# Optimization experiments

Hardware: AMD Instinct MI355X
Metric: run time of the kernel (lower is better)

## Reference

```python
import jax, jax.numpy as jnp
import numpy as np

N = 4194304  # batch of 2-D points
N_NODE = 16
N_INT = 5


def setup_inputs() -> dict:
    key = jax.random.key(0)
    k1, k2, k3, k4 = jax.random.split(key, 4)
    # Kaiming-ish small init so ReLU chain doesn't blow up
    x = jax.random.normal(k1, (N, 2), dtype=jnp.float32)
    w_in = jax.random.normal(k2, (N_NODE, 2), dtype=jnp.float32) * (1.0 / np.sqrt(2.0))
    w_mid = jax.random.normal(k3, (N_INT, N_NODE, N_NODE), dtype=jnp.float32) * (1.0 / np.sqrt(N_NODE))
    w_out = jax.random.normal(k4, (2, N_NODE), dtype=jnp.float32) * (1.0 / np.sqrt(N_NODE))
    return {"x": x, "w_in": w_in, "w_mid": w_mid, "w_out": w_out}


def reference(x, w_in, w_mid, w_out):
    # Linear(2,16,bias=False) + ReLU
    h = jax.nn.relu(x @ w_in.T)  # [N, 16]
    def step(h, w):
        return jax.nn.relu(h @ w.T), None
    h, _ = jax.lax.scan(step, h, w_mid)
    # final Linear(16,2,bias=False), no activation
    return h @ w_out.T  # [N, 2]
```

## Files before the change

kernel.cpp:

```cpp
#include <hip/hip_runtime.h>


typedef _Float16 h8 __attribute__((ext_vector_type(8)));
typedef float f16v __attribute__((ext_vector_type(16)));
typedef float f4 __attribute__((ext_vector_type(4)));
typedef float f2 __attribute__((ext_vector_type(2)));
typedef unsigned int u32;
typedef u32 u4v __attribute__((ext_vector_type(4)));

static __device__ __forceinline__ f16v mfma32(h8 a, h8 b, f16v c) {
    return __builtin_amdgcn_mfma_f32_32x32x16_f16(a, b, c, 0, 0, 0);
}

static __device__ __forceinline__ u32 cvtpk(float a, float b) {
    return __builtin_bit_cast(u32, __builtin_amdgcn_cvt_pkrtz(a, b));
}

static __device__ __forceinline__ h8 pack4(u32 a, u32 b, u32 c, u32 d) {
    u4v p = {a, b, c, d};
    return __builtin_bit_cast(h8, p);
}

static __device__ __forceinline__ h8 wfrag(const float* row, int hi) {
    const f4* r4 = (const f4*)row;
    f4 q0 = r4[hi], q1 = r4[hi + 2];
    return pack4(cvtpk(q0.x, q0.y), cvtpk(q0.z, q0.w),
                 cvtpk(q1.x, q1.y), cvtpk(q1.z, q1.w));
}

static __device__ __forceinline__ h8 cvt_relu8(f16v a) {
    h8 hb = pack4(cvtpk(a[0], a[1]), cvtpk(a[2], a[3]),
                  cvtpk(a[4], a[5]), cvtpk(a[6], a[7]));
    const h8 z = {};
    return __builtin_elementwise_max(hb, z);
}

__global__ __launch_bounds__(256, 4) void denoiser_mfma32(
    const f2* __restrict__ x,
    const float* __restrict__ w_in,
    const float* __restrict__ w_mid,
    const float* __restrict__ w_out,
    f2* __restrict__ out,
    int n)
{
    const int lane = threadIdx.x & 63;
    const int m    = lane & 15;
    const int hi   = lane >> 5;
    const int wave = threadIdx.x >> 6;

    const h8 hz = {};

    u32 wxy = cvtpk(w_in[2 * m], w_in[2 * m + 1]);
    h8 wi0 = hi == 0 ? pack4(wxy, 0u, 0u, 0u) : hz;
    h8 wi1 = hi == 1 ? pack4(wxy, 0u, 0u, 0u) : hz;

    h8 wm0 = wfrag(w_mid + 0 * 256 + m * 16, hi);
    h8 wm1 = wfrag(w_mid + 1 * 256 + m * 16, hi);
    h8 wm2 = wfrag(w_mid + 2 * 256 + m * 16, hi);
    h8 wm3 = wfrag(w_mid + 3 * 256 + m * 16, hi);
    h8 wm4 = wfrag(w_mid + 4 * 256 + m * 16, hi);

    h8 wo = m < 2 ? wfrag(w_out + m * 16, hi) : hz;

    f16v z16 = {};
    asm("" : "+v"(z16));

    const int nchunks = (n + 255) >> 8;
    const int stride  = gridDim.x;
    const int nm1     = n - 1;

    auto loadx = [&](int c) -> f2 {
        int pi = c * 256 + wave * 64 + lane;
        return x[pi < n ? pi : nm1];
    };

    auto stream = [&](h8 wi, h8 bin, int sbase) {
        f16v a = mfma32(wi, bin, z16);
        h8 b = cvt_relu8(a);
        a = mfma32(wm0, b, z16);  b = cvt_relu8(a);
        a = mfma32(wm1, b, z16);  b = cvt_relu8(a);
        a = mfma32(wm2, b, z16);  b = cvt_relu8(a);
        a = mfma32(wm3, b, z16);  b = cvt_relu8(a);
        a = mfma32(wm4, b, z16);  b = cvt_relu8(a);
        a = mfma32(wo, b, z16);

        if (lane < 32) {
            int p0 = sbase + lane;
            if (p0 < n) out[p0] = (f2){a[0], a[1]};
        }
    };

    auto body = [&](int c, f2 xy) {
        const int base = c * 256 + wave * 64;
        h8 bin = pack4(cvtpk(xy.x, xy.y), 0u, 0u, 0u);
        stream(wi0, bin, base);
        stream(wi1, bin, base + 32);
    };

    int c = blockIdx.x;
    f2 xyA = loadx(c);
    f2 xyB = loadx(c + stride < nchunks ? c + stride : c);

    for (; c < nchunks; c += 2 * stride) {
        const int cB  = c + stride;
        const int cA2 = c + 2 * stride;
        const int cB2 = c + 3 * stride;

        f2 xyA2 = loadx(cA2 < nchunks ? cA2 : c);
        f2 xyB2 = loadx(cB2 < nchunks ? cB2 : c);

        body(c, xyA);
        if (cB < nchunks) body(cB, xyB);

        xyA = xyA2;
        xyB = xyB2;
    }
}

extern "C" void kernel_launch(void* const* d_in, const int* in_sizes, int n_in,
                              void* d_out, int out_size, void* d_ws, size_t ws_size,
                              hipStream_t stream) {
    const float* x     = (const float*)d_in[0];
    const float* w_in  = (const float*)d_in[1];
    const float* w_mid = (const float*)d_in[2];
    const float* w_out = (const float*)d_in[3];

    int n = in_sizes[0] / 2;
    int nchunks = (n + 255) / 256;
    int blocks = nchunks < 2048 ? nchunks : 2048;

    denoiser_mfma32<<<blocks, 256, 0, stream>>>(
        (const f2*)x, w_in, w_mid, w_out, (f2*)d_out, n);
}
```

Before: 33.98 us.

## Replace grid-stride prefetch loop with one chunk per block launch

```diff
diff --git a/kernel.cpp b/kernel.cpp
--- a/kernel.cpp
+++ b/kernel.cpp
@@ -65,16 +65,16 @@
     f16v z16 = {};
     asm("" : "+v"(z16));
 
-    const int nchunks = (n + 255) >> 8;
-    const int stride  = gridDim.x;
-    const int nm1     = n - 1;
+    const int base = blockIdx.x * 256 + wave * 64;
 
-    auto loadx = [&](int c) -> f2 {
-        int pi = c * 256 + wave * 64 + lane;
-        return x[pi < n ? pi : nm1];
-    };
+    f2 xy;
+    {
+        int pi = base + lane;
+        xy = x[pi < n ? pi : n - 1];
+    }
+    h8 bin = pack4(cvtpk(xy.x, xy.y), 0u, 0u, 0u);
 
-    auto stream = [&](h8 wi, h8 bin, int sbase) {
+    auto stream = [&](h8 wi, int sbase) {
         f16v a = mfma32(wi, bin, z16);
         h8 b = cvt_relu8(a);
         a = mfma32(wm0, b, z16);  b = cvt_relu8(a);
@@ -90,31 +90,8 @@
         }
     };
 
-    auto body = [&](int c, f2 xy) {
-        const int base = c * 256 + wave * 64;
-        h8 bin = pack4(cvtpk(xy.x, xy.y), 0u, 0u, 0u);
-        stream(wi0, bin, base);
-        stream(wi1, bin, base + 32);
-    };
-
-    int c = blockIdx.x;
-    f2 xyA = loadx(c);
-    f2 xyB = loadx(c + stride < nchunks ? c + stride : c);
-
-    for (; c < nchunks; c += 2 * stride) {
-        const int cB  = c + stride;
-        const int cA2 = c + 2 * stride;
-        const int cB2 = c + 3 * stride;
-
-        f2 xyA2 = loadx(cA2 < nchunks ? cA2 : c);
-        f2 xyB2 = loadx(cB2 < nchunks ? cB2 : c);
-
-        body(c, xyA);
-        if (cB < nchunks) body(cB, xyB);
-
-        xyA = xyA2;
-        xyB = xyB2;
-    }
+    stream(wi0, base);
+    stream(wi1, base + 32);
 }
 
 extern "C" void kernel_launch(void* const* d_in, const int* in_sizes, int n_in,
@@ -126,8 +103,7 @@
     const float* w_out = (const float*)d_in[3];
 
     int n = in_sizes[0] / 2;
-    int nchunks = (n + 255) / 256;
-    int blocks = nchunks < 2048 ? nchunks : 2048;
+    int blocks = (n + 255) / 256;
 
     denoiser_mfma32<<<blocks, 256, 0, stream>>>(
         (const f2*)x, w_in, w_mid, w_out, (f2*)d_out, n);
```

New measurement: 51.87 us. 52.6% more time.

## Switch to 16x16x32 MFMA with four independent point streams per wave

Applied to the files above, without the earlier changes.

```diff
diff --git a/kernel.cpp b/kernel.cpp
--- a/kernel.cpp
+++ b/kernel.cpp
@@ -2,14 +2,15 @@
 
 
 typedef _Float16 h8 __attribute__((ext_vector_type(8)));
-typedef float f16v __attribute__((ext_vector_type(16)));
+typedef _Float16 h4v __attribute__((ext_vector_type(4)));
 typedef float f4 __attribute__((ext_vector_type(4)));
 typedef float f2 __attribute__((ext_vector_type(2)));
 typedef unsigned int u32;
+typedef u32 u2v __attribute__((ext_vector_type(2)));
 typedef u32 u4v __attribute__((ext_vector_type(4)));
 
-static __device__ __forceinline__ f16v mfma32(h8 a, h8 b, f16v c) {
-    return __builtin_amdgcn_mfma_f32_32x32x16_f16(a, b, c, 0, 0, 0);
+static __device__ __forceinline__ f4 mfma32k(h8 a, h8 b, f4 c) {
+    return __builtin_amdgcn_mfma_f32_16x16x32_f16(a, b, c, 0, 0, 0);
 }
 
 static __device__ __forceinline__ u32 cvtpk(float a, float b) {
@@ -21,21 +22,22 @@
     return __builtin_bit_cast(h8, p);
 }
 
-static __device__ __forceinline__ h8 wfrag(const float* row, int hi) {
+static __device__ __forceinline__ h8 wfrag(const float* row, int g) {
     const f4* r4 = (const f4*)row;
-    f4 q0 = r4[hi], q1 = r4[hi + 2];
-    return pack4(cvtpk(q0.x, q0.y), cvtpk(q0.z, q0.w),
-                 cvtpk(q1.x, q1.y), cvtpk(q1.z, q1.w));
+    f4 q = r4[g];
+    return pack4(cvtpk(q.x, q.y), cvtpk(q.z, q.w), 0u, 0u);
 }
 
-static __device__ __forceinline__ h8 cvt_relu8(f16v a) {
-    h8 hb = pack4(cvtpk(a[0], a[1]), cvtpk(a[2], a[3]),
-                  cvtpk(a[4], a[5]), cvtpk(a[6], a[7]));
-    const h8 z = {};
-    return __builtin_elementwise_max(hb, z);
+static __device__ __forceinline__ h8 cvt_relu4(f4 a) {
+    u2v c = { cvtpk(a[0], a[1]), cvtpk(a[2], a[3]) };
+    h4v hb = __builtin_bit_cast(h4v, c);
+    const h4v z = {};
+    hb = __builtin_elementwise_max(hb, z);
+    u2v r = __builtin_bit_cast(u2v, hb);
+    return pack4(r.x, r.y, 0u, 0u);
 }
 
-__global__ __launch_bounds__(256, 4) void denoiser_mfma32(
+__global__ __launch_bounds__(256, 4) void denoiser_mfma16k32(
     const f2* __restrict__ x,
     const float* __restrict__ w_in,
     const float* __restrict__ w_mid,
@@ -44,26 +46,34 @@
     int n)
 {
     const int lane = threadIdx.x & 63;
-    const int m    = lane & 15;
-    const int hi   = lane >> 5;
+    const int nn   = lane & 15;
+    const int g    = lane >> 4;
     const int wave = threadIdx.x >> 6;
 
     const h8 hz = {};
 
-    u32 wxy = cvtpk(w_in[2 * m], w_in[2 * m + 1]);
-    h8 wi0 = hi == 0 ? pack4(wxy, 0u, 0u, 0u) : hz;
-    h8 wi1 = hi == 1 ? pack4(wxy, 0u, 0u, 0u) : hz;
+    u32 wxy = cvtpk(w_in[2 * nn], w_in[2 * nn + 1]);
+    h8 wiv = pack4(wxy, 0u, 0u, 0u);
+    h8 wi0 = g == 0 ? wiv : hz;
+    h8 wi1 = g == 1 ? wiv : hz;
+    h8 wi2 = g == 2 ? wiv : hz;
+    h8 wi3 = g == 3 ? wiv : hz;
 
-    h8 wm0 = wfrag(w_mid + 0 * 256 + m * 16, hi);
-    h8 wm1 = wfrag(w_mid + 1 * 256 + m * 16, hi);
-    h8 wm2 = wfrag(w_mid + 2 * 256 + m * 16, hi);
-    h8 wm3 = wfrag(w_mid + 3 * 256 + m * 16, hi);
-    h8 wm4 = wfrag(w_mid + 4 * 256 + m * 16, hi);
+    h8 wm0 = wfrag(w_mid + 0 * 256 + nn * 16, g);
+    h8 wm1 = wfrag(w_mid + 1 * 256 + nn * 16, g);
+    h8 wm2 = wfrag(w_mid + 2 * 256 + nn * 16, g);
+    h8 wm3 = wfrag(w_mid + 3 * 256 + nn * 16, g);
+    h8 wm4 = wfrag(w_mid + 4 * 256 + nn * 16, g);
 
-    h8 wo = m < 2 ? wfrag(w_out + m * 16, hi) : hz;
+    h8 wofull = (nn & 3) < 2 ? wfrag(w_out + (nn & 3) * 16, g) : hz;
+    int tsel = nn >> 2;
+    h8 wo0 = tsel == 0 ? wofull : hz;
+    h8 wo1 = tsel == 1 ? wofull : hz;
+    h8 wo2 = tsel == 2 ? wofull : hz;
+    h8 wo3 = tsel == 3 ? wofull : hz;
 
-    f16v z16 = {};
-    asm("" : "+v"(z16));
+    f4 z4 = {};
+    asm("" : "+v"(z4));
 
     const int nchunks = (n + 255) >> 8;
     const int stride  = gridDim.x;
@@ -74,46 +84,57 @@
         return x[pi < n ? pi : nm1];
     };
 
-    auto stream = [&](h8 wi, h8 bin, int sbase) {
-        f16v a = mfma32(wi, bin, z16);
-        h8 b = cvt_relu8(a);
-        a = mfma32(wm0, b, z16);  b = cvt_relu8(a);
-        a = mfma32(wm1, b, z16);  b = cvt_relu8(a);
-        a = mfma32(wm2, b, z16);  b = cvt_relu8(a);
-        a = mfma32(wm3, b, z16);  b = cvt_relu8(a);
-        a = mfma32(wm4, b, z16);  b = cvt_relu8(a);
-        a = mfma32(wo, b, z16);
-
-        if (lane < 32) {
-            int p0 = sbase + lane;
-            if (p0 < n) out[p0] = (f2){a[0], a[1]};
-        }
-    };
-
-    auto body = [&](int c, f2 xy) {
-        const int base = c * 256 + wave * 64;
-        h8 bin = pack4(cvtpk(xy.x, xy.y), 0u, 0u, 0u);
-        stream(wi0, bin, base);
-        stream(wi1, bin, base + 32);
+    auto selstore = [&](f4 a0, f4 a1, f4 a2, f4 a3) -> f2 {
+        float s0 = g < 2 ? (g == 1 ? a1[0] : a0[0]) : (g == 3 ? a3[0] : a2[0]);
+        float s1 = g < 2 ? (g == 1 ? a1[1] : a0[1]) : (g == 3 ? a3[1] : a2[1]);
+        return (f2){s0, s1};
     };
 
     int c = blockIdx.x;
-    f2 xyA = loadx(c);
-    f2 xyB = loadx(c + stride < nchunks ? c + stride : c);
+    f2 xy = loadx(c);
 
-    for (; c < nchunks; c += 2 * stride) {
-        const int cB  = c + stride;
-        const int cA2 = c + 2 * stride;
-        const int cB2 = c + 3 * stride;
+    for (; c < nchunks; c += stride) {
+        const int cn = c + stride;
+        f2 xyn = loadx(cn < nchunks ? cn : c);
 
-        f2 xyA2 = loadx(cA2 < nchunks ? cA2 : c);
-        f2 xyB2 = loadx(cB2 < nchunks ? cB2 : c);
+        const int base = c * 256 + wave * 64;
 
-        body(c, xyA);
-        if (cB < nchunks) body(cB, xyB);
+        h8 bin = pack4(cvtpk(xy.x, xy.y), 0u, 0u, 0u);
+        f4 a0 = mfma32k(wi0, bin, z4);
+        f4 a1 = mfma32k(wi1, bin, z4);
+        f4 a2 = mfma32k(wi2, bin, z4);
+        f4 a3 = mfma32k(wi3, bin, z4);
+        h8 b0 = cvt_relu4(a0);
+        h8 b1 = cvt_relu4(a1);
+        h8 b2 = cvt_relu4(a2);
+        h8 b3 = cvt_relu4(a3);
 
-        xyA = xyA2;
-        xyB = xyB2;
+        #define MIDLAYER(W)                                      \
+            a0 = mfma32k(W, b0, z4);  a1 = mfma32k(W, b1, z4);   \
+            a2 = mfma32k(W, b2, z4);  a3 = mfma32k(W, b3, z4);   \
+            b0 = cvt_relu4(a0);  b1 = cvt_relu4(a1);             \
+            b2 = cvt_relu4(a2);  b3 = cvt_relu4(a3);
+        MIDLAYER(wm0)
+        MIDLAYER(wm1)
+        MIDLAYER(wm2)
+        MIDLAYER(wm3)
+        MIDLAYER(wm4)
+        #undef MIDLAYER
+
+        a0 = mfma32k(wo0, b0, z4);
+        a1 = mfma32k(wo1, b1, z4);
+        a2 = mfma32k(wo2, b2, z4);
+        a3 = mfma32k(wo3, b3, z4);
+
+        f2 o = selstore(a0, a1, a2, a3);
+
+        if (base + 64 <= n) {
+            out[base + lane] = o;
+        } else if (base + lane < n) {
+            out[base + lane] = o;
+        }
+
+        xy = xyn;
     }
 }
 
@@ -129,6 +150,6 @@
     int nchunks = (n + 255) / 256;
     int blocks = nchunks < 2048 ? nchunks : 2048;
 
-    denoiser_mfma32<<<blocks, 256, 0, stream>>>(
+    denoiser_mfma16k32<<<blocks, 256, 0, stream>>>(
         (const f2*)x, w_in, w_mid, w_out, (f2*)d_out, n);
 }
```

Result: slower. 36.05 us (+6.1%).
